# Kernel optimization log

Measured on AMD Instinct MI355X. Metric: run time of the kernel, lower is better.

The kernel has to match this reference:

```python
import jax, jax.numpy as jnp
import numpy as np

B = 8          # graphs per batch
N_PER = 8192   # nodes per graph (equal-sized graphs -> static topk shapes)
N = B * N_PER  # 65536 total nodes
DEG = 16
E = DEG * N    # 1,048,576 edges
C = 64         # conv_width


def setup_inputs() -> dict:
    key = jax.random.key(0)
    ks = jax.random.split(key, 32)
    epg = E // B
    g = jnp.arange(E, dtype=jnp.int32) // epg            # graph id per edge
    src = jax.random.randint(ks[0], (E,), 0, N_PER, dtype=jnp.int32) + g * N_PER
    dst = jax.random.randint(ks[1], (E,), 0, N_PER, dtype=jnp.int32) + g * N_PER

    def w(k, shape, fan_in):
        return (jax.random.normal(k, shape) / np.sqrt(fan_in)).astype(jnp.float32)

    inp = {
        "x": jax.random.normal(ks[2], (N, 2), dtype=jnp.float32),
        "edge_index": jnp.stack([src, dst]),
        # SAGEConv i: out = mean_agg @ wl + x @ wr + b
        "w1l": w(ks[3], (2, C), 2),  "w1r": w(ks[4], (2, C), 2),  "b1": jnp.zeros((C,), jnp.float32),
        "w2l": w(ks[5], (C, C), C),  "w2r": w(ks[6], (C, C), C),  "b2": jnp.zeros((C,), jnp.float32),
        "w3l": w(ks[7], (C, C), C),  "w3r": w(ks[8], (C, C), C),  "b3": jnp.zeros((C,), jnp.float32),
        # GCNConv
        "w4": w(ks[9], (C, C), C),   "b4": jnp.zeros((C,), jnp.float32),
        # TopKPooling score vectors
        "p1": w(ks[10], (C,), C), "p2": w(ks[11], (C,), C),
        "p3": w(ks[12], (C,), C), "p4": w(ks[13], (C,), C),
        # MLP head
        "lw1": w(ks[14], (2 * C, 128), 2 * C), "lb1": jnp.zeros((128,), jnp.float32),
        "lw2": w(ks[15], (128, 64), 128),      "lb2": jnp.zeros((64,), jnp.float32),
        "lw3": w(ks[16], (64, 1), 64),         "lb3": jnp.zeros((1,), jnp.float32),
    }
    return inp


def _sage(x, src, dst, em, wl, wr, b):
    # PyG SAGEConv: lin_l(mean of in-neighbors) + lin_r(x); masked edges contribute 0
    n = x.shape[0]
    s = jax.ops.segment_sum(x[src] * em[:, None], dst, num_segments=n)
    cnt = jax.ops.segment_sum(em, dst, num_segments=n)
    mean = s / jnp.maximum(cnt, 1.0)[:, None]
    return mean @ wl + x @ wr + b


def _gcn(x, src, dst, em, w, b):
    # PyG GCNConv with added self-loops, symmetric normalization
    n = x.shape[0]
    xw = x @ w
    deg = jax.ops.segment_sum(em, dst, num_segments=n) + 1.0  # +1 self-loop
    dinv = jax.lax.rsqrt(deg)
    coef = (dinv[src] * dinv[dst] * em)[:, None]
    agg = jax.ops.segment_sum(xw[src] * coef, dst, num_segments=n)
    return agg + xw / deg[:, None] + b  # self-loop term: deg^-0.5 * deg^-0.5


def _pool(x, src, dst, em, p, nb):
    # TopKPooling(ratio=0.5): score = x.p/||p||, keep top half per graph, scale by tanh
    n = x.shape[0]
    npg = n // nb
    k = npg // 2
    score = x @ p / jnp.linalg.norm(p)
    _, idx = jax.lax.top_k(score.reshape(nb, npg), k)          # [nb, k] local idx
    perm = (idx + (jnp.arange(nb, dtype=idx.dtype) * npg)[:, None]).reshape(-1)
    xn = x[perm] * jnp.tanh(score[perm])[:, None]
    o2n = jnp.full((n,), -1, jnp.int32).at[perm].set(jnp.arange(nb * k, dtype=jnp.int32))
    ns, nd = o2n[src], o2n[dst]
    nm = em * ((ns >= 0) & (nd >= 0)).astype(em.dtype)         # filter_adj via mask
    return xn, jnp.maximum(ns, 0), jnp.maximum(nd, 0), nm


def _readout(x, nb):
    # cat([global_max_pool, global_mean_pool])
    npg = x.shape[0] // nb
    batch = jnp.repeat(jnp.arange(nb), npg)
    mx = jax.ops.segment_max(x, batch, num_segments=nb)
    mn = jax.ops.segment_sum(x, batch, num_segments=nb) / npg
    return jnp.concatenate([mx, mn], axis=1)


def reference(x, edge_index, w1l, w1r, b1, w2l, w2r, b2, w3l, w3r, b3, w4, b4,
              p1, p2, p3, p4, lw1, lb1, lw2, lb2, lw3, lb3):
    src, dst = edge_index[0], edge_index[1]
    em = jnp.ones((src.shape[0],), jnp.float32)

    h = jax.nn.relu(_sage(x, src, dst, em, w1l, w1r, b1))
    h, src, dst, em = _pool(h, src, dst, em, p1, B)
    x1 = _readout(h, B)

    h = jax.nn.relu(_sage(h, src, dst, em, w2l, w2r, b2))
    h, src, dst, em = _pool(h, src, dst, em, p2, B)
    x2 = _readout(h, B)

    h = jax.nn.relu(_sage(h, src, dst, em, w3l, w3r, b3))
    h, src, dst, em = _pool(h, src, dst, em, p3, B)
    x3 = _readout(h, B)  # computed but unused, matching original (x = x1 + x2)

    h = jax.nn.relu(_gcn(h, src, dst, em, w4, b4))
    h, src, dst, em = _pool(h, src, dst, em, p4, B)
    x4 = _readout(h, B)  # computed but unused, matching original

    z = x1 + x2
    z = jax.nn.relu(z @ lw1 + lb1)
    z = jax.nn.relu(z @ lw2 + lb2)
    return z @ lw3 + lb3  # [B, 1]
```

## Files before the change

### kernel.cpp

```cpp
#include <hip/hip_runtime.h>
#include <stdint.h>
#include <math.h>

#define NB 8
#define NPG0 8192
#define EPG 131072
#define P1 16
#define MAXDEG 64

__global__ __launch_bounds__(1024)
void k_aggp(const int* __restrict__ src, const int* __restrict__ dst,
            const float* __restrict__ x, float* __restrict__ partial)
{
    __shared__ float acc[3 * 2048];
    int b = blockIdx.x;
    int g = b >> 6, qq = (b >> 4) & 3, sl = b & 15;
    int tid = threadIdx.x;
    float4* acc4 = (float4*)acc;
    float4 z4 = make_float4(0.f, 0.f, 0.f, 0.f);
    acc4[tid] = z4;
    if (tid < 512) acc4[1024 + tid] = z4;
    __syncthreads();
    int e0 = g * EPG + sl * (EPG / P1);
    int nbase = g * NPG0 + qq * 2048;
    const float2* x2 = reinterpret_cast<const float2*>(x);
    #pragma unroll
    for (int k = 0; k < 2; ++k) {
        int e = e0 + (k * 1024 + tid) * 4;
        int4 d4 = *reinterpret_cast<const int4*>(dst + e);
        unsigned l0 = (unsigned)(d4.x - nbase), l1 = (unsigned)(d4.y - nbase);
        unsigned l2 = (unsigned)(d4.z - nbase), l3 = (unsigned)(d4.w - nbase);
        bool v0 = l0 < 2048u, v1 = l1 < 2048u, v2 = l2 < 2048u, v3 = l3 < 2048u;
        if (v0 | v1 | v2 | v3) {
            int4 s4 = *reinterpret_cast<const int4*>(src + e);
            if (v0) { float2 xv = x2[s4.x]; atomicAdd(&acc[l0], xv.x);
                      atomicAdd(&acc[2048 + l0], xv.y); atomicAdd(&acc[4096 + l0], 1.0f); }
            if (v1) { float2 xv = x2[s4.y]; atomicAdd(&acc[l1], xv.x);
                      atomicAdd(&acc[2048 + l1], xv.y); atomicAdd(&acc[4096 + l1], 1.0f); }
            if (v2) { float2 xv = x2[s4.z]; atomicAdd(&acc[l2], xv.x);
                      atomicAdd(&acc[2048 + l2], xv.y); atomicAdd(&acc[4096 + l2], 1.0f); }
            if (v3) { float2 xv = x2[s4.w]; atomicAdd(&acc[l3], xv.x);
                      atomicAdd(&acc[2048 + l3], xv.y); atomicAdd(&acc[4096 + l3], 1.0f); }
        }
    }
    __syncthreads();
    float4* o = (float4*)(partial + (size_t)b * 6144);
    o[tid] = acc4[tid];
    if (tid < 512) o[1024 + tid] = acc4[1024 + tid];
}

__global__ __launch_bounds__(256)
void k_sage1f(const float* __restrict__ partial, const float* __restrict__ x,
              const float* __restrict__ w1l, const float* __restrict__ w1r,
              const float* __restrict__ b1, const float* __restrict__ p1,
              float4* __restrict__ mvx, float* __restrict__ th,
              float* __restrict__ s1)
{
    int tid = threadIdx.x;
    int node = blockIdx.x * 256 + tid;
    int g = node >> 13, local = node & (NPG0 - 1);
    int qq = local >> 11, ll = local & 2047;
    const float* p = partial + (size_t)(g * 64 + qq * 16) * 6144 + ll;
    float s0 = 0.f, s1v = 0.f, sc = 0.f;
    #pragma unroll
    for (int q = 0; q < 16; ++q) {
        const float* pq = p + (size_t)q * 6144;
        s0 += pq[0]; s1v += pq[2048]; sc += pq[4096];
    }
    float inv = 1.0f / fmaxf(sc, 1.0f);
    float m0 = s0 * inv, m1 = s1v * inv;
    float2 xv = reinterpret_cast<const float2*>(x)[node];
    mvx[node] = make_float4(m0, m1, xv.x, xv.y);
    float num = 0.f, nrm = 0.f;
    #pragma unroll 8
    for (int c = 0; c < 64; ++c) {
        float h = fmaxf(m0 * w1l[c] + m1 * w1l[64 + c]
                      + xv.x * w1r[c] + xv.y * w1r[64 + c] + b1[c], 0.0f);
        float pv = p1[c];
        num += h * pv; nrm += pv * pv;
    }
    float score = num / sqrtf(nrm);
    s1[node] = score;
    th[node] = tanhf(score);
}

__device__ __forceinline__ unsigned scan1024(unsigned val, volatile unsigned* ws)
{
    int tid = threadIdx.x, lane = tid & 63, wid = tid >> 6;
    unsigned sc = val;
    #pragma unroll
    for (int off = 1; off < 64; off <<= 1) {
        unsigned t = __shfl_up(sc, off);
        if (lane >= off) sc += t;
    }
    if (lane == 63) ws[wid] = sc;
    __syncthreads();
    if (tid < 16) {
        unsigned w = ws[tid];
        #pragma unroll
        for (int off = 1; off < 16; off <<= 1) {
            unsigned t = __shfl_up(w, off);
            if (tid >= off) w += t;
        }
        ws[tid] = w;
    }
    __syncthreads();
    return sc + (wid ? ws[wid - 1] : 0u);
}

__global__ __launch_bounds__(1024)
void k_pool1(const float* __restrict__ score, int* __restrict__ n2o,
             int* __restrict__ o2n, int K, int* __restrict__ zbuf)
{
    const int NPG = 8192;
    __shared__ unsigned key[NPG];
    __shared__ unsigned hist[1024];
    __shared__ unsigned ws[16];
    __shared__ unsigned long long cand[1024];
    __shared__ int sT1, sR1, sT2, sR2, selCnt, c3;
    int g = blockIdx.x, tid = threadIdx.x;
    for (int i = tid; i < 4096; i += 1024) zbuf[g * 4096 + i] = 0;
    if (tid == 0) { selCnt = 0; c3 = 0; }
    hist[tid] = 0u;
    for (int i = tid; i < NPG; i += 1024) o2n[g * NPG + i] = -1;
    __syncthreads();
    for (int i = tid; i < NPG; i += 1024) {
        unsigned b = __float_as_uint(score[g * NPG + i]);
        unsigned u = (b & 0x80000000u) ? ~b : (b | 0x80000000u);
        key[i] = u;
        atomicAdd(&hist[u >> 22], 1u);
    }
    __syncthreads();
    {
        unsigned S = scan1024(hist[1023 - tid], ws);
        int b = 1023 - tid;
        unsigned h = hist[b];
        if (S >= (unsigned)K && S - h < (unsigned)K) { sT1 = b; sR1 = K - (int)(S - h); }
    }
    __syncthreads();
    int T1 = sT1, R1 = sR1;
    for (int i = tid; i < NPG; i += 1024) {
        if ((int)(key[i] >> 22) > T1) {
            int s = atomicAdd(&selCnt, 1);
            int oldid = g * NPG + i;
            n2o[g * K + s] = oldid;
            o2n[oldid] = g * K + s;
        }
    }
    __syncthreads();
    hist[tid] = 0u;
    __syncthreads();
    for (int i = tid; i < NPG; i += 1024)
        if ((int)(key[i] >> 22) == T1) atomicAdd(&hist[(key[i] >> 12) & 1023u], 1u);
    __syncthreads();
    {
        unsigned S = scan1024(hist[1023 - tid], ws);
        int b = 1023 - tid;
        unsigned h = hist[b];
        if (S >= (unsigned)R1 && S - h < (unsigned)R1) { sT2 = b; sR2 = R1 - (int)(S - h); }
    }
    __syncthreads();
    int T2 = sT2, R2 = sR2;
    for (int i = tid; i < NPG; i += 1024) {
        unsigned u = key[i];
        if ((int)(u >> 22) == T1) {
            int b2 = (int)((u >> 12) & 1023u);
            if (b2 > T2) {
                int s = atomicAdd(&selCnt, 1);
                int oldid = g * NPG + i;
                n2o[g * K + s] = oldid;
                o2n[oldid] = g * K + s;
            } else if (b2 == T2) {
                int c = atomicAdd(&c3, 1);
                if (c < 1024)
                    cand[c] = ((unsigned long long)u << 32) | (unsigned)(NPG - 1 - i);
            }
        }
    }
    __syncthreads();
    int M = min(c3, 1024);
    for (int t = tid; t < M; t += 1024) {
        unsigned long long k0 = cand[t];
        int rank = 0;
        for (int j = 0; j < M; ++j) rank += (cand[j] > k0);
        if (rank < R2) {
            int i = NPG - 1 - (int)(k0 & 0xFFFFFFFFu);
            int s = atomicAdd(&selCnt, 1);
            int oldid = g * NPG + i;
            n2o[g * K + s] = oldid;
            o2n[oldid] = g * K + s;
        }
    }
}

__global__ __launch_bounds__(1024)
void k_pool2(const float* __restrict__ score, int* __restrict__ n2o, int K)
{
    const int NPG = 4096;
    __shared__ unsigned key[NPG];
    __shared__ unsigned hist[1024];
    __shared__ unsigned ws[16];
    __shared__ unsigned long long cand[1024];
    __shared__ int sT1, sR1, sT2, sR2, selCnt, c3;
    int g = blockIdx.x, tid = threadIdx.x;
    if (tid == 0) { selCnt = 0; c3 = 0; }
    hist[tid] = 0u;
    __syncthreads();
    for (int i = tid; i < NPG; i += 1024) {
        unsigned b = __float_as_uint(score[g * NPG + i]);
        unsigned u = (b & 0x80000000u) ? ~b : (b | 0x80000000u);
        key[i] = u;
        atomicAdd(&hist[u >> 22], 1u);
    }
    __syncthreads();
    {
        unsigned S = scan1024(hist[1023 - tid], ws);
        int b = 1023 - tid;
        unsigned h = hist[b];
        if (S >= (unsigned)K && S - h < (unsigned)K) { sT1 = b; sR1 = K - (int)(S - h); }
    }
    __syncthreads();
    int T1 = sT1, R1 = sR1;
    for (int i = tid; i < NPG; i += 1024) {
        if ((int)(key[i] >> 22) > T1)
            n2o[g * K + atomicAdd(&selCnt, 1)] = g * NPG + i;
    }
    __syncthreads();
    hist[tid] = 0u;
    __syncthreads();
    for (int i = tid; i < NPG; i += 1024)
        if ((int)(key[i] >> 22) == T1) atomicAdd(&hist[(key[i] >> 12) & 1023u], 1u);
    __syncthreads();
    {
        unsigned S = scan1024(hist[1023 - tid], ws);
        int b = 1023 - tid;
        unsigned h = hist[b];
        if (S >= (unsigned)R1 && S - h < (unsigned)R1) { sT2 = b; sR2 = R1 - (int)(S - h); }
    }
    __syncthreads();
    int T2 = sT2, R2 = sR2;
    for (int i = tid; i < NPG; i += 1024) {
        unsigned u = key[i];
        if ((int)(u >> 22) == T1) {
            int b2 = (int)((u >> 12) & 1023u);
            if (b2 > T2) {
                n2o[g * K + atomicAdd(&selCnt, 1)] = g * NPG + i;
            } else if (b2 == T2) {
                int c = atomicAdd(&c3, 1);
                if (c < 1024)
                    cand[c] = ((unsigned long long)u << 32) | (unsigned)(NPG - 1 - i);
            }
        }
    }
    __syncthreads();
    int M = min(c3, 1024);
    for (int t = tid; t < M; t += 1024) {
        unsigned long long k0 = cand[t];
        int rank = 0;
        for (int j = 0; j < M; ++j) rank += (cand[j] > k0);
        if (rank < R2) {
            int i = NPG - 1 - (int)(k0 & 0xFFFFFFFFu);
            n2o[g * K + atomicAdd(&selCnt, 1)] = g * NPG + i;
        }
    }
}

__global__ __launch_bounds__(1024)
void k_mid(const float4* __restrict__ mvx, const float* __restrict__ th,
           const int* __restrict__ n2o,
           const float* __restrict__ w1l, const float* __restrict__ w1r,
           const float* __restrict__ b1, int npg,
           float* __restrict__ pmx, float* __restrict__ psm,
           const int* __restrict__ src, const int* __restrict__ dst,
           const int* __restrict__ o2n, int* __restrict__ cnt,
           int* __restrict__ slots)
{
    __shared__ float4 smx[1024], ssm[1024];
    int b = blockIdx.x;
    int tid = threadIdx.x;
    if (b >= 128) {
        int e = ((b - 128) * 1024 + tid) * 4;
        int4 s4 = *reinterpret_cast<const int4*>(src + e);
        int4 d4 = *reinterpret_cast<const int4*>(dst + e);
        #pragma unroll
        for (int i = 0; i < 4; ++i) {
            int sv = (i == 0) ? s4.x : (i == 1) ? s4.y : (i == 2) ? s4.z : s4.w;
            int dv = (i == 0) ? d4.x : (i == 1) ? d4.y : (i == 2) ? d4.z : d4.w;
            int ns = o2n[sv], nd = o2n[dv];
            if (ns >= 0 && nd >= 0) {
                int pos = atomicAdd(&cnt[nd], 1);
                if (pos < MAXDEG) slots[nd * MAXDEG + pos] = sv;
            }
        }
        return;
    }
    int g = b >> 4, sl = b & 15;
    int cg = tid & 15, rsl = tid >> 4;
    int rpb = npg >> 4;
    int c0 = cg * 4;
    float4 wl0 = *reinterpret_cast<const float4*>(w1l + c0);
    float4 wl1 = *reinterpret_cast<const float4*>(w1l + 64 + c0);
    float4 wr0 = *reinterpret_cast<const float4*>(w1r + c0);
    float4 wr1 = *reinterpret_cast<const float4*>(w1r + 64 + c0);
    float4 bb  = *reinterpret_cast<const float4*>(b1 + c0);
    float4 mx = make_float4(-INFINITY, -INFINITY, -INFINITY, -INFINITY);
    float4 sm = make_float4(0.f, 0.f, 0.f, 0.f);
    for (int r = rsl; r < rpb; r += 64) {
        int row = g * npg + sl * rpb + r;
        int old = n2o[row];
        float4 m = mvx[old];
        float t = th[old];
        float4 v;
        v.x = fmaxf(m.x * wl0.x + m.y * wl1.x + m.z * wr0.x + m.w * wr1.x + bb.x, 0.f) * t;
        v.y = fmaxf(m.x * wl0.y + m.y * wl1.y + m.z * wr0.y + m.w * wr1.y + bb.y, 0.f) * t;
        v.z = fmaxf(m.x * wl0.z + m.y * wl1.z + m.z * wr0.z + m.w * wr1.z + bb.z, 0.f) * t;
        v.w = fmaxf(m.x * wl0.w + m.y * wl1.w + m.z * wr0.w + m.w * wr1.w + bb.w, 0.f) * t;
        mx.x = fmaxf(mx.x, v.x); mx.y = fmaxf(mx.y, v.y);
        mx.z = fmaxf(mx.z, v.z); mx.w = fmaxf(mx.w, v.w);
        sm.x += v.x; sm.y += v.y; sm.z += v.z; sm.w += v.w;
    }
    smx[tid] = mx; ssm[tid] = sm;
    __syncthreads();
    for (int s = 32; s >= 1; s >>= 1) {
        if (rsl < s) {
            float4 a = smx[tid], bq = smx[tid + s * 16];
            a.x = fmaxf(a.x, bq.x); a.y = fmaxf(a.y, bq.y);
            a.z = fmaxf(a.z, bq.z); a.w = fmaxf(a.w, bq.w);
            smx[tid] = a;
            float4 c = ssm[tid], d = ssm[tid + s * 16];
            c.x += d.x; c.y += d.y; c.z += d.z; c.w += d.w;
            ssm[tid] = c;
        }
        __syncthreads();
    }
    if (rsl == 0) {
        reinterpret_cast<float4*>(pmx)[(g * 16 + sl) * 16 + cg] = smx[tid];
        reinterpret_cast<float4*>(psm)[(g * 16 + sl) * 16 + cg] = ssm[tid];
    }
}

__global__ __launch_bounds__(256)
void k_sage2(const float4* __restrict__ mvx, const float* __restrict__ th,
             const int* __restrict__ n2o, const int* __restrict__ cnt,
             const int* __restrict__ slots,
             const float* __restrict__ w1l, const float* __restrict__ w1r,
             const float* __restrict__ b1,
             const float* __restrict__ w2l, const float* __restrict__ w2r,
             const float* __restrict__ b2, const float* __restrict__ p2,
             float* __restrict__ h2, float* __restrict__ s2)
{
    __shared__ float Xs[64 * 128];
    __shared__ float Wt[64 * 128];
    int tid = threadIdx.x, blk = blockIdx.x;

    #pragma unroll
    for (int i = 0; i < 32; ++i) {
        int idx = i * 256 + tid;
        int k = idx >> 6, c = idx & 63;
        float w = (k < 64) ? w2l[k * 64 + c] : w2r[(k - 64) * 64 + c];
        int slot = (k >> 2) ^ ((c >> 2) & 7);
        Wt[c * 128 + slot * 4 + (k & 3)] = w;
    }

    {
        int n = tid >> 2, p = tid & 3;
        int j = blk * 64 + n;
        int dg = cnt[j];
        int lim = min(dg, MAXDEG);
        const int* sl = slots + j * MAXDEG;
        float4 wl0[4], wl1[4], wr0[4], wr1[4], bb[4];
        #pragma unroll
        for (int u = 0; u < 4; ++u) {
            int c = p * 16 + u * 4;
            wl0[u] = *reinterpret_cast<const float4*>(w1l + c);
            wl1[u] = *reinterpret_cast<const float4*>(w1l + 64 + c);
            wr0[u] = *reinterpret_cast<const float4*>(w1r + c);
            wr1[u] = *reinterpret_cast<const float4*>(w1r + 64 + c);
            bb[u]  = *reinterpret_cast<const float4*>(b1 + c);
        }
        auto hfun = [&](const float4& m, float t, int u) -> float4 {
            float4 r;
            r.x = fmaxf(m.x * wl0[u].x + m.y * wl1[u].x + m.z * wr0[u].x + m.w * wr1[u].x + bb[u].x, 0.f) * t;
            r.y = fmaxf(m.x * wl0[u].y + m.y * wl1[u].y + m.z * wr0[u].y + m.w * wr1[u].y + bb[u].y, 0.f) * t;
            r.z = fmaxf(m.x * wl0[u].z + m.y * wl1[u].z + m.z * wr0[u].z + m.w * wr1[u].z + bb[u].z, 0.f) * t;
            r.w = fmaxf(m.x * wl0[u].w + m.y * wl1[u].w + m.z * wr0[u].w + m.w * wr1[u].w + bb[u].w, 0.f) * t;
            return r;
        };
        float4 a[4];
        #pragma unroll
        for (int u = 0; u < 4; ++u) a[u] = make_float4(0.f, 0.f, 0.f, 0.f);
        int e = 0;
        for (; e + 1 < lim; e += 2) {
            int o0 = sl[e], o1 = sl[e + 1];
            float4 mA = mvx[o0]; float tA = th[o0];
            float4 mB = mvx[o1]; float tB = th[o1];
            #pragma unroll
            for (int u = 0; u < 4; ++u) {
                float4 vA = hfun(mA, tA, u), vB = hfun(mB, tB, u);
                a[u].x += vA.x + vB.x; a[u].y += vA.y + vB.y;
                a[u].z += vA.z + vB.z; a[u].w += vA.w + vB.w;
            }
        }
        if (e < lim) {
            int o0 = sl[e];
            float4 mA = mvx[o0]; float tA = th[o0];
            #pragma unroll
            for (int u = 0; u < 4; ++u) {
                float4 vA = hfun(mA, tA, u);
                a[u].x += vA.x; a[u].y += vA.y; a[u].z += vA.z; a[u].w += vA.w;
            }
        }
        float inv = 1.0f / fmaxf((float)dg, 1.0f);
        int swz = (n >> 2) & 7;
        float4* X4 = reinterpret_cast<float4*>(Xs);
        #pragma unroll
        for (int u = 0; u < 4; ++u) {
            float4 m = a[u];
            m.x *= inv; m.y *= inv; m.z *= inv; m.w *= inv;
            X4[n * 32 + ((p * 4 + u) ^ swz)] = m;
        }
        int os = n2o[j];
        float4 mS = mvx[os]; float tS = th[os];
        #pragma unroll
        for (int u = 0; u < 4; ++u)
            X4[n * 32 + ((16 + p * 4 + u) ^ swz)] = hfun(mS, tS, u);
    }
    __syncthreads();

    int rt = tid >> 4, ct = tid & 15;
    int r0 = rt * 4, c0 = ct * 4;
    int swa = rt & 7, swb = ct & 7;
    const float4* Xf = reinterpret_cast<const float4*>(Xs);
    const float4* Wf = reinterpret_cast<const float4*>(Wt);
    float acc[4][4];
    #pragma unroll
    for (int i = 0; i < 4; ++i)
        #pragma unroll
        for (int jq = 0; jq < 4; ++jq) acc[i][jq] = 0.f;
    #pragma unroll 8
    for (int ks = 0; ks < 32; ++ks) {
        float4 aa[4], bb[4];
        #pragma unroll
        for (int i = 0; i < 4; ++i) aa[i] = Xf[(r0 + i) * 32 + (ks ^ swa)];
        #pragma unroll
        for (int jq = 0; jq < 4; ++jq) bb[jq] = Wf[(c0 + jq) * 32 + (ks ^ swb)];
        #pragma unroll
        for (int i = 0; i < 4; ++i)
            #pragma unroll
            for (int jq = 0; jq < 4; ++jq)
                acc[i][jq] += aa[i].x * bb[jq].x + aa[i].y * bb[jq].y
                            + aa[i].z * bb[jq].z + aa[i].w * bb[jq].w;
    }

    float4 b2v = reinterpret_cast<const float4*>(b2)[ct];
    float4 p2v = reinterpret_cast<const float4*>(p2)[ct];
    float nrm = p2v.x * p2v.x + p2v.y * p2v.y + p2v.z * p2v.z + p2v.w * p2v.w;
    float sp[4];
    float4* h2f = reinterpret_cast<float4*>(h2);
    #pragma unroll
    for (int i = 0; i < 4; ++i) {
        float4 o;
        o.x = fmaxf(acc[i][0] + b2v.x, 0.f);
        o.y = fmaxf(acc[i][1] + b2v.y, 0.f);
        o.z = fmaxf(acc[i][2] + b2v.z, 0.f);
        o.w = fmaxf(acc[i][3] + b2v.w, 0.f);
        h2f[(blk * 64 + r0 + i) * 16 + ct] = o;
        sp[i] = o.x * p2v.x + o.y * p2v.y + o.z * p2v.z + o.w * p2v.w;
    }
    #pragma unroll
    for (int o = 1; o < 16; o <<= 1) {
        #pragma unroll
        for (int i = 0; i < 4; ++i) sp[i] += __shfl_xor(sp[i], o);
        nrm += __shfl_xor(nrm, o);
    }
    if (ct == 0) {
        float r = rsqrtf(nrm);
        #pragma unroll
        for (int i = 0; i < 4; ++i) s2[blk * 64 + r0 + i] = sp[i] * r;
    }
}

__global__ __launch_bounds__(1024)
void k_readout_p(const float* __restrict__ h, const int* __restrict__ n2o,
                 const float* __restrict__ sc, int npg,
                 float* __restrict__ pmx, float* __restrict__ psm)
{
    int g = blockIdx.x >> 4, sl = blockIdx.x & 15;
    int tid = threadIdx.x;
    int cg = tid & 15, rsl = tid >> 4;
    int rpb = npg >> 4;
    float4 mx = make_float4(-INFINITY, -INFINITY, -INFINITY, -INFINITY);
    float4 sm = make_float4(0.f, 0.f, 0.f, 0.f);
    for (int r = rsl; r < rpb; r += 64) {
        int row = g * npg + sl * rpb + r;
        int oldid = n2o[row];
        float t = tanhf(sc[oldid]);
        float4 v = reinterpret_cast<const float4*>(h)[oldid * 16 + cg];
        v.x *= t; v.y *= t; v.z *= t; v.w *= t;
        mx.x = fmaxf(mx.x, v.x); mx.y = fmaxf(mx.y, v.y);
        mx.z = fmaxf(mx.z, v.z); mx.w = fmaxf(mx.w, v.w);
        sm.x += v.x; sm.y += v.y; sm.z += v.z; sm.w += v.w;
    }
    __shared__ float4 smx[1024], ssm[1024];
    smx[tid] = mx; ssm[tid] = sm;
    __syncthreads();
    for (int s = 32; s >= 1; s >>= 1) {
        if (rsl < s) {
            float4 a = smx[tid], b = smx[tid + s * 16];
            a.x = fmaxf(a.x, b.x); a.y = fmaxf(a.y, b.y);
            a.z = fmaxf(a.z, b.z); a.w = fmaxf(a.w, b.w);
            smx[tid] = a;
            float4 c = ssm[tid], d = ssm[tid + s * 16];
            c.x += d.x; c.y += d.y; c.z += d.z; c.w += d.w;
            ssm[tid] = c;
        }
        __syncthreads();
    }
    if (rsl == 0) {
        reinterpret_cast<float4*>(pmx)[(g * 16 + sl) * 16 + cg] = smx[tid];
        reinterpret_cast<float4*>(psm)[(g * 16 + sl) * 16 + cg] = ssm[tid];
    }
}

__global__ __launch_bounds__(128)
void k_mlp(const float* __restrict__ pmx1, const float* __restrict__ psm1,
           const float* __restrict__ pmx2, const float* __restrict__ psm2,
           int npg1, int npg2,
           const float* __restrict__ lw1, const float* __restrict__ lb1,
           const float* __restrict__ lw2, const float* __restrict__ lb2,
           const float* __restrict__ lw3, const float* __restrict__ lb3,
           float* __restrict__ out)
{
    __shared__ float z[NB][128], o1[NB][128], o2[NB][64];
    int tid = threadIdx.x;
    for (int g = 0; g < NB; ++g) {
        float v;
        if (tid < 64) {
            float m1 = -INFINITY, m2 = -INFINITY;
            #pragma unroll
            for (int sl = 0; sl < 16; ++sl) {
                m1 = fmaxf(m1, pmx1[(g * 16 + sl) * 64 + tid]);
                m2 = fmaxf(m2, pmx2[(g * 16 + sl) * 64 + tid]);
            }
            v = m1 + m2;
        } else {
            int ch = tid - 64;
            float s1 = 0.f, s2 = 0.f;
            #pragma unroll
            for (int sl = 0; sl < 16; ++sl) {
                s1 += psm1[(g * 16 + sl) * 64 + ch];
                s2 += psm2[(g * 16 + sl) * 64 + ch];
            }
            v = s1 / (float)npg1 + s2 / (float)npg2;
        }
        z[g][tid] = v;
    }
    __syncthreads();
    {
        float a[NB];
        #pragma unroll
        for (int g = 0; g < NB; ++g) a[g] = lb1[tid];
        for (int i = 0; i < 128; ++i) {
            float wv = lw1[i * 128 + tid];
            #pragma unroll
            for (int g = 0; g < NB; ++g) a[g] += z[g][i] * wv;
        }
        #pragma unroll
        for (int g = 0; g < NB; ++g) o1[g][tid] = fmaxf(a[g], 0.0f);
    }
    __syncthreads();
    if (tid < 64) {
        float a[NB];
        #pragma unroll
        for (int g = 0; g < NB; ++g) a[g] = lb2[tid];
        for (int i = 0; i < 128; ++i) {
            float wv = lw2[i * 64 + tid];
            #pragma unroll
            for (int g = 0; g < NB; ++g) a[g] += o1[g][i] * wv;
        }
        #pragma unroll
        for (int g = 0; g < NB; ++g) o2[g][tid] = fmaxf(a[g], 0.0f);
    }
    __syncthreads();
    if (tid < NB) {
        int g = tid;
        float a = lb3[0];
        for (int i = 0; i < 64; ++i) a += o2[g][i] * lw3[i];
        out[g] = a;
    }
}

extern "C" void kernel_launch(void* const* d_in, const int* in_sizes, int n_in,
                              void* d_out, int out_size, void* d_ws, size_t ws_size,
                              hipStream_t stream)
{
    (void)n_in; (void)out_size; (void)ws_size;
    const float* x   = (const float*)d_in[0];
    const int*   ei  = (const int*)d_in[1];
    const float* w1l = (const float*)d_in[2];
    const float* w1r = (const float*)d_in[3];
    const float* b1  = (const float*)d_in[4];
    const float* w2l = (const float*)d_in[5];
    const float* w2r = (const float*)d_in[6];
    const float* b2  = (const float*)d_in[7];
    const float* p1  = (const float*)d_in[13];
    const float* p2  = (const float*)d_in[14];
    const float* lw1 = (const float*)d_in[17];
    const float* lb1 = (const float*)d_in[18];
    const float* lw2 = (const float*)d_in[19];
    const float* lb2 = (const float*)d_in[20];
    const float* lw3 = (const float*)d_in[21];
    const float* lb3 = (const float*)d_in[22];

    const int N0   = in_sizes[0] / 2;
    const int E    = in_sizes[1] / 2;
    const int K1   = NPG0 / 2;
    const int N1   = NB * K1;
    const int K2   = K1 / 2;

    const int* src = ei;
    const int* dst = ei + E;

    char* w = (char*)d_ws;
    auto alloc = [&](size_t bytes) -> char* {
        char* p = w;
        w += (bytes + 255) & ~(size_t)255;
        return p;
    };
    float*  partial = (float*)alloc((size_t)NB * 4 * P1 * 6144 * 4);
    float4* mvx   = (float4*)alloc((size_t)N0 * 16);
    float*  th    = (float*)alloc((size_t)N0 * 4);
    int*    cnt2  = (int*)alloc((size_t)N1 * 4);
    int*    slots = (int*)alloc((size_t)N1 * MAXDEG * 4);
    float*  s1    = (float*)alloc((size_t)N0 * 4);
    int*    o2n1  = (int*)alloc((size_t)N0 * 4);
    int*    n2o1  = (int*)alloc((size_t)N1 * 4);
    float*  h2    = (float*)alloc((size_t)N1 * 64 * 4);
    float*  s2    = (float*)alloc((size_t)N1 * 4);
    int*    n2o2  = (int*)alloc((size_t)(NB * K2) * 4);
    float*  pmx1  = (float*)alloc((size_t)NB * 16 * 64 * 4);
    float*  psm1  = (float*)alloc((size_t)NB * 16 * 64 * 4);
    float*  pmx2  = (float*)alloc((size_t)NB * 16 * 64 * 4);
    float*  psm2  = (float*)alloc((size_t)NB * 16 * 64 * 4);

    k_aggp<<<NB * 4 * P1, 1024, 0, stream>>>(src, dst, x, partial);
    k_sage1f<<<N0 / 256, 256, 0, stream>>>(partial, x, w1l, w1r, b1, p1, mvx, th, s1);
    k_pool1<<<NB, 1024, 0, stream>>>(s1, n2o1, o2n1, K1, cnt2);
    k_mid<<<128 + 256, 1024, 0, stream>>>(mvx, th, n2o1, w1l, w1r, b1, K1,
                                          pmx1, psm1,
                                          src, dst, o2n1, cnt2, slots);
    k_sage2<<<N1 / 64, 256, 0, stream>>>(mvx, th, n2o1, cnt2, slots,
                                         w1l, w1r, b1, w2l, w2r, b2, p2, h2, s2);
    k_pool2<<<NB, 1024, 0, stream>>>(s2, n2o2, K2);
    k_readout_p<<<NB * 16, 1024, 0, stream>>>(h2, n2o2, s2, K2, pmx2, psm2);
    k_mlp<<<1, 128, 0, stream>>>(pmx1, psm1, pmx2, psm2, K1, K2,
                                 lw1, lb1, lw2, lb2, lw3, lb3, (float*)d_out);
}
```

Baseline: 121.0 us.

## Fuse second pooling, readout and MLP head into one per-graph kernel

Merges k_pool2, k_readout_p and k_mlp into a single kernel with one 1024-thread block per graph. Selected indices stay in shared memory instead of going through a global n2o array, the readout reduction uses wave shuffles, and each block runs the MLP for its own graph. This removes two launches and the global round trips between them. In exchange the readout now runs on only 8 blocks instead of 128, so the gather of h2 rows has much less parallelism.

```diff
diff --git a/kernel.cpp b/kernel.cpp
--- a/kernel.cpp
+++ b/kernel.cpp
@@ -189,78 +189,6 @@
             int oldid = g * NPG + i;
             n2o[g * K + s] = oldid;
             o2n[oldid] = g * K + s;
-        }
-    }
-}
-
-__global__ __launch_bounds__(1024)
-void k_pool2(const float* __restrict__ score, int* __restrict__ n2o, int K)
-{
-    const int NPG = 4096;
-    __shared__ unsigned key[NPG];
-    __shared__ unsigned hist[1024];
-    __shared__ unsigned ws[16];
-    __shared__ unsigned long long cand[1024];
-    __shared__ int sT1, sR1, sT2, sR2, selCnt, c3;
-    int g = blockIdx.x, tid = threadIdx.x;
-    if (tid == 0) { selCnt = 0; c3 = 0; }
-    hist[tid] = 0u;
-    __syncthreads();
-    for (int i = tid; i < NPG; i += 1024) {
-        unsigned b = __float_as_uint(score[g * NPG + i]);
-        unsigned u = (b & 0x80000000u) ? ~b : (b | 0x80000000u);
-        key[i] = u;
-        atomicAdd(&hist[u >> 22], 1u);
-    }
-    __syncthreads();
-    {
-        unsigned S = scan1024(hist[1023 - tid], ws);
-        int b = 1023 - tid;
-        unsigned h = hist[b];
-        if (S >= (unsigned)K && S - h < (unsigned)K) { sT1 = b; sR1 = K - (int)(S - h); }
-    }
-    __syncthreads();
-    int T1 = sT1, R1 = sR1;
-    for (int i = tid; i < NPG; i += 1024) {
-        if ((int)(key[i] >> 22) > T1)
-            n2o[g * K + atomicAdd(&selCnt, 1)] = g * NPG + i;
-    }
-    __syncthreads();
-    hist[tid] = 0u;
-    __syncthreads();
-    for (int i = tid; i < NPG; i += 1024)
-        if ((int)(key[i] >> 22) == T1) atomicAdd(&hist[(key[i] >> 12) & 1023u], 1u);
-    __syncthreads();
-    {
-        unsigned S = scan1024(hist[1023 - tid], ws);
-        int b = 1023 - tid;
-        unsigned h = hist[b];
-        if (S >= (unsigned)R1 && S - h < (unsigned)R1) { sT2 = b; sR2 = R1 - (int)(S - h); }
-    }
-    __syncthreads();
-    int T2 = sT2, R2 = sR2;
-    for (int i = tid; i < NPG; i += 1024) {
-        unsigned u = key[i];
-        if ((int)(u >> 22) == T1) {
-            int b2 = (int)((u >> 12) & 1023u);
-            if (b2 > T2) {
-                n2o[g * K + atomicAdd(&selCnt, 1)] = g * NPG + i;
-            } else if (b2 == T2) {
-                int c = atomicAdd(&c3, 1);
-                if (c < 1024)
-                    cand[c] = ((unsigned long long)u << 32) | (unsigned)(NPG - 1 - i);
-            }
-        }
-    }
-    __syncthreads();
-    int M = min(c3, 1024);
-    for (int t = tid; t < M; t += 1024) {
-        unsigned long long k0 = cand[t];
-        int rank = 0;
-        for (int j = 0; j < M; ++j) rank += (cand[j] > k0);
-        if (rank < R2) {
-            int i = NPG - 1 - (int)(k0 & 0xFFFFFFFFu);
-            n2o[g * K + atomicAdd(&selCnt, 1)] = g * NPG + i;
         }
     }
 }
@@ -481,111 +409,155 @@
 }
 
 __global__ __launch_bounds__(1024)
-void k_readout_p(const float* __restrict__ h, const int* __restrict__ n2o,
-                 const float* __restrict__ sc, int npg,
-                 float* __restrict__ pmx, float* __restrict__ psm)
-{
-    int g = blockIdx.x >> 4, sl = blockIdx.x & 15;
-    int tid = threadIdx.x;
-    int cg = tid & 15, rsl = tid >> 4;
-    int rpb = npg >> 4;
+void k_tail2(const float* __restrict__ s2, const float* __restrict__ h2,
+             const float* __restrict__ pmx1, const float* __restrict__ psm1,
+             const float* __restrict__ lw1, const float* __restrict__ lb1,
+             const float* __restrict__ lw2, const float* __restrict__ lb2,
+             const float* __restrict__ lw3, const float* __restrict__ lb3,
+             float* __restrict__ out)
+{
+    const int NPG = 4096, K = 2048;
+    __shared__ unsigned key[NPG];
+    __shared__ unsigned hist[1024];
+    __shared__ unsigned ws[16];
+    __shared__ unsigned long long cand[1024];
+    __shared__ int sel[K];
+    __shared__ float4 wmx[256], wsm[256];
+    __shared__ float zbuf[128], o1b[128], o2b[64];
+    __shared__ int sT1, sR1, sT2, sR2, selCnt, c3;
+    int g = blockIdx.x, tid = threadIdx.x;
+
+    if (tid == 0) { selCnt = 0; c3 = 0; }
+    hist[tid] = 0u;
+    __syncthreads();
+    for (int i = tid; i < NPG; i += 1024) {
+        unsigned b = __float_as_uint(s2[g * NPG + i]);
+        unsigned u = (b & 0x80000000u) ? ~b : (b | 0x80000000u);
+        key[i] = u;
+        atomicAdd(&hist[u >> 22], 1u);
+    }
+    __syncthreads();
+    {
+        unsigned S = scan1024(hist[1023 - tid], ws);
+        int b = 1023 - tid;
+        unsigned h = hist[b];
+        if (S >= (unsigned)K && S - h < (unsigned)K) { sT1 = b; sR1 = K - (int)(S - h); }
+    }
+    __syncthreads();
+    int T1 = sT1, R1 = sR1;
+    for (int i = tid; i < NPG; i += 1024) {
+        if ((int)(key[i] >> 22) > T1) sel[atomicAdd(&selCnt, 1)] = i;
+    }
+    __syncthreads();
+    hist[tid] = 0u;
+    __syncthreads();
+    for (int i = tid; i < NPG; i += 1024)
+        if ((int)(key[i] >> 22) == T1) atomicAdd(&hist[(key[i] >> 12) & 1023u], 1u);
+    __syncthreads();
+    {
+        unsigned S = scan1024(hist[1023 - tid], ws);
+        int b = 1023 - tid;
+        unsigned h = hist[b];
+        if (S >= (unsigned)R1 && S - h < (unsigned)R1) { sT2 = b; sR2 = R1 - (int)(S - h); }
+    }
+    __syncthreads();
+    int T2 = sT2, R2 = sR2;
+    for (int i = tid; i < NPG; i += 1024) {
+        unsigned u = key[i];
+        if ((int)(u >> 22) == T1) {
+            int b2 = (int)((u >> 12) & 1023u);
+            if (b2 > T2) {
+                sel[atomicAdd(&selCnt, 1)] = i;
+            } else if (b2 == T2) {
+                int c = atomicAdd(&c3, 1);
+                if (c < 1024)
+                    cand[c] = ((unsigned long long)u << 32) | (unsigned)(NPG - 1 - i);
+            }
+        }
+    }
+    __syncthreads();
+    int M = min(c3, 1024);
+    for (int t = tid; t < M; t += 1024) {
+        unsigned long long k0 = cand[t];
+        int rank = 0;
+        for (int j = 0; j < M; ++j) rank += (cand[j] > k0);
+        if (rank < R2) sel[atomicAdd(&selCnt, 1)] = NPG - 1 - (int)(k0 & 0xFFFFFFFFu);
+    }
+    __syncthreads();
+
+    int cg = tid & 15;
     float4 mx = make_float4(-INFINITY, -INFINITY, -INFINITY, -INFINITY);
     float4 sm = make_float4(0.f, 0.f, 0.f, 0.f);
-    for (int r = rsl; r < rpb; r += 64) {
-        int row = g * npg + sl * rpb + r;
-        int oldid = n2o[row];
-        float t = tanhf(sc[oldid]);
-        float4 v = reinterpret_cast<const float4*>(h)[oldid * 16 + cg];
-        v.x *= t; v.y *= t; v.z *= t; v.w *= t;
-        mx.x = fmaxf(mx.x, v.x); mx.y = fmaxf(mx.y, v.y);
-        mx.z = fmaxf(mx.z, v.z); mx.w = fmaxf(mx.w, v.w);
-        sm.x += v.x; sm.y += v.y; sm.z += v.z; sm.w += v.w;
-    }
-    __shared__ float4 smx[1024], ssm[1024];
-    smx[tid] = mx; ssm[tid] = sm;
-    __syncthreads();
-    for (int s = 32; s >= 1; s >>= 1) {
-        if (rsl < s) {
-            float4 a = smx[tid], b = smx[tid + s * 16];
-            a.x = fmaxf(a.x, b.x); a.y = fmaxf(a.y, b.y);
-            a.z = fmaxf(a.z, b.z); a.w = fmaxf(a.w, b.w);
-            smx[tid] = a;
-            float4 c = ssm[tid], d = ssm[tid + s * 16];
-            c.x += d.x; c.y += d.y; c.z += d.z; c.w += d.w;
-            ssm[tid] = c;
-        }
-        __syncthreads();
-    }
-    if (rsl == 0) {
-        reinterpret_cast<float4*>(pmx)[(g * 16 + sl) * 16 + cg] = smx[tid];
-        reinterpret_cast<float4*>(psm)[(g * 16 + sl) * 16 + cg] = ssm[tid];
-    }
-}
-
-__global__ __launch_bounds__(128)
-void k_mlp(const float* __restrict__ pmx1, const float* __restrict__ psm1,
-           const float* __restrict__ pmx2, const float* __restrict__ psm2,
-           int npg1, int npg2,
-           const float* __restrict__ lw1, const float* __restrict__ lb1,
-           const float* __restrict__ lw2, const float* __restrict__ lb2,
-           const float* __restrict__ lw3, const float* __restrict__ lb3,
-           float* __restrict__ out)
-{
-    __shared__ float z[NB][128], o1[NB][128], o2[NB][64];
-    int tid = threadIdx.x;
-    for (int g = 0; g < NB; ++g) {
-        float v;
-        if (tid < 64) {
-            float m1 = -INFINITY, m2 = -INFINITY;
-            #pragma unroll
-            for (int sl = 0; sl < 16; ++sl) {
-                m1 = fmaxf(m1, pmx1[(g * 16 + sl) * 64 + tid]);
-                m2 = fmaxf(m2, pmx2[(g * 16 + sl) * 64 + tid]);
-            }
-            v = m1 + m2;
-        } else {
-            int ch = tid - 64;
-            float s1 = 0.f, s2 = 0.f;
-            #pragma unroll
-            for (int sl = 0; sl < 16; ++sl) {
-                s1 += psm1[(g * 16 + sl) * 64 + ch];
-                s2 += psm2[(g * 16 + sl) * 64 + ch];
-            }
-            v = s1 / (float)npg1 + s2 / (float)npg2;
-        }
-        z[g][tid] = v;
-    }
-    __syncthreads();
     {
-        float a[NB];
-        #pragma unroll
-        for (int g = 0; g < NB; ++g) a[g] = lb1[tid];
-        for (int i = 0; i < 128; ++i) {
-            float wv = lw1[i * 128 + tid];
-            #pragma unroll
-            for (int g = 0; g < NB; ++g) a[g] += z[g][i] * wv;
-        }
-        #pragma unroll
-        for (int g = 0; g < NB; ++g) o1[g][tid] = fmaxf(a[g], 0.0f);
-    }
-    __syncthreads();
+        int rsl = tid >> 4;
+        for (int r = rsl; r < K; r += 64) {
+            int old = g * NPG + sel[r];
+            float t = tanhf(s2[old]);
+            float4 v = reinterpret_cast<const float4*>(h2)[old * 16 + cg];
+            v.x *= t; v.y *= t; v.z *= t; v.w *= t;
+            mx.x = fmaxf(mx.x, v.x); mx.y = fmaxf(mx.y, v.y);
+            mx.z = fmaxf(mx.z, v.z); mx.w = fmaxf(mx.w, v.w);
+            sm.x += v.x; sm.y += v.y; sm.z += v.z; sm.w += v.w;
+        }
+    }
+    #pragma unroll
+    for (int o = 16; o <= 32; o <<= 1) {
+        mx.x = fmaxf(mx.x, __shfl_xor(mx.x, o));
+        mx.y = fmaxf(mx.y, __shfl_xor(mx.y, o));
+        mx.z = fmaxf(mx.z, __shfl_xor(mx.z, o));
+        mx.w = fmaxf(mx.w, __shfl_xor(mx.w, o));
+        sm.x += __shfl_xor(sm.x, o); sm.y += __shfl_xor(sm.y, o);
+        sm.z += __shfl_xor(sm.z, o); sm.w += __shfl_xor(sm.w, o);
+    }
+    {
+        int lane = tid & 63, wid = tid >> 6;
+        if (lane < 16) { wmx[wid * 16 + cg] = mx; wsm[wid * 16 + cg] = sm; }
+    }
+    __syncthreads();
+    if (tid < 16) {
+        float4 Mv = wmx[tid], Sv = wsm[tid];
+        for (int w2 = 1; w2 < 16; ++w2) {
+            float4 a = wmx[w2 * 16 + tid], b = wsm[w2 * 16 + tid];
+            Mv.x = fmaxf(Mv.x, a.x); Mv.y = fmaxf(Mv.y, a.y);
+            Mv.z = fmaxf(Mv.z, a.z); Mv.w = fmaxf(Mv.w, a.w);
+            Sv.x += b.x; Sv.y += b.y; Sv.z += b.z; Sv.w += b.w;
+        }
+        wmx[tid] = Mv; wsm[tid] = Sv;
+    }
+    __syncthreads();
+
     if (tid < 64) {
-        float a[NB];
-        #pragma unroll
-        for (int g = 0; g < NB; ++g) a[g] = lb2[tid];
-        for (int i = 0; i < 128; ++i) {
-            float wv = lw2[i * 64 + tid];
-            #pragma unroll
-            for (int g = 0; g < NB; ++g) a[g] += o1[g][i] * wv;
-        }
-        #pragma unroll
-        for (int g = 0; g < NB; ++g) o2[g][tid] = fmaxf(a[g], 0.0f);
-    }
-    __syncthreads();
-    if (tid < NB) {
-        int g = tid;
+        float m1 = -INFINITY;
+        #pragma unroll
+        for (int s = 0; s < 16; ++s)
+            m1 = fmaxf(m1, pmx1[(g * 16 + s) * 64 + tid]);
+        zbuf[tid] = m1 + reinterpret_cast<const float*>(wmx)[tid];
+    } else if (tid < 128) {
+        int ch = tid - 64;
+        float a1 = 0.f;
+        #pragma unroll
+        for (int s = 0; s < 16; ++s)
+            a1 += psm1[(g * 16 + s) * 64 + ch];
+        zbuf[tid] = a1 / 4096.0f
+                  + reinterpret_cast<const float*>(wsm)[ch] / 2048.0f;
+    }
+    __syncthreads();
+
+    if (tid < 128) {
+        float a = lb1[tid];
+        for (int i = 0; i < 128; ++i) a += zbuf[i] * lw1[i * 128 + tid];
+        o1b[tid] = fmaxf(a, 0.0f);
+    }
+    __syncthreads();
+    if (tid < 64) {
+        float a = lb2[tid];
+        for (int i = 0; i < 128; ++i) a += o1b[i] * lw2[i * 64 + tid];
+        o2b[tid] = fmaxf(a, 0.0f);
+    }
+    __syncthreads();
+    if (tid == 0) {
         float a = lb3[0];
-        for (int i = 0; i < 64; ++i) a += o2[g][i] * lw3[i];
+        for (int i = 0; i < 64; ++i) a += o2b[i] * lw3[i];
         out[g] = a;
     }
 }
@@ -616,7 +588,6 @@
     const int E    = in_sizes[1] / 2;
     const int K1   = NPG0 / 2;
     const int N1   = NB * K1;
-    const int K2   = K1 / 2;
 
     const int* src = ei;
     const int* dst = ei + E;
@@ -637,11 +608,8 @@
     int*    n2o1  = (int*)alloc((size_t)N1 * 4);
     float*  h2    = (float*)alloc((size_t)N1 * 64 * 4);
     float*  s2    = (float*)alloc((size_t)N1 * 4);
-    int*    n2o2  = (int*)alloc((size_t)(NB * K2) * 4);
     float*  pmx1  = (float*)alloc((size_t)NB * 16 * 64 * 4);
     float*  psm1  = (float*)alloc((size_t)NB * 16 * 64 * 4);
-    float*  pmx2  = (float*)alloc((size_t)NB * 16 * 64 * 4);
-    float*  psm2  = (float*)alloc((size_t)NB * 16 * 64 * 4);
 
     k_aggp<<<NB * 4 * P1, 1024, 0, stream>>>(src, dst, x, partial);
     k_sage1f<<<N0 / 256, 256, 0, stream>>>(partial, x, w1l, w1r, b1, p1, mvx, th, s1);
@@ -651,8 +619,6 @@
                                           src, dst, o2n1, cnt2, slots);
     k_sage2<<<N1 / 64, 256, 0, stream>>>(mvx, th, n2o1, cnt2, slots,
                                          w1l, w1r, b1, w2l, w2r, b2, p2, h2, s2);
-    k_pool2<<<NB, 1024, 0, stream>>>(s2, n2o2, K2);
-    k_readout_p<<<NB * 16, 1024, 0, stream>>>(h2, n2o2, s2, K2, pmx2, psm2);
-    k_mlp<<<1, 128, 0, stream>>>(pmx1, psm1, pmx2, psm2, K1, K2,
-                                 lw1, lb1, lw2, lb2, lw3, lb3, (float*)d_out);
-}
+    k_tail2<<<NB, 1024, 0, stream>>>(s2, h2, pmx1, psm1,
+                                     lw1, lb1, lw2, lb2, lw3, lb3, (float*)d_out);
+}
```

Result: no change. 121.0 us (median of 2 runs) (-0.0%).
